# Performance work log

Measured on AMD Instinct MI355X. Metric: run time of the kernel, lower is better.

Reference implementation:

```python
import jax, jax.numpy as jnp
import numpy as np

EMBED_DIM = 1024
NUM_HEADS = 16
HEAD_DIM = EMBED_DIM // NUM_HEADS


def setup_inputs() -> dict:
    key = jax.random.key(0)
    ks = jax.random.split(key, 5)
    s = 0.02
    return {
        "x": jax.random.normal(ks[0], (2, 2048, EMBED_DIM), dtype=jnp.float32),
        "w_qkv": jax.random.normal(ks[1], (EMBED_DIM, 3 * EMBED_DIM), dtype=jnp.float32) * s,
        "b_qkv": jnp.zeros((3 * EMBED_DIM,), dtype=jnp.float32),
        "w_out": jax.random.normal(ks[2], (EMBED_DIM, EMBED_DIM), dtype=jnp.float32) * s,
        "b_out": jnp.zeros((EMBED_DIM,), dtype=jnp.float32),
    }


def reference(x, w_qkv, b_qkv, w_out, b_out):
    B, T, C = x.shape
    qkv = x @ w_qkv + b_qkv                       # [B,T,3C]
    q, k, v = jnp.split(qkv, 3, axis=-1)
    # [B,T,C] -> [B,H,T,Dh]
    def heads(t):
        return t.reshape(B, T, NUM_HEADS, HEAD_DIM).transpose(0, 2, 1, 3)
    q, k, v = heads(q), heads(k), heads(v)
    scale = 1.0 / np.sqrt(HEAD_DIM).astype(np.float32)
    scores = jnp.einsum("bhqd,bhkd->bhqk", q, k) * scale  # [B,H,T,T]
    causal = jnp.tril(jnp.ones((T, T), dtype=bool))
    scores = jnp.where(causal[None, None], scores, -jnp.inf)
    attn = jax.nn.softmax(scores, axis=-1)
    out = jnp.einsum("bhqk,bhkd->bhqd", attn, v)  # [B,H,T,Dh]
    out = out.transpose(0, 2, 1, 3).reshape(B, T, C)
    return out @ w_out + b_out
```

## Files before the change

kernel.cpp:

```cpp
#include <hip/hip_runtime.h>

typedef unsigned short u16;
typedef unsigned int u32;
typedef __attribute__((ext_vector_type(8))) short bf16x8;
typedef __attribute__((ext_vector_type(4))) float f32x4;
typedef __attribute__((ext_vector_type(16))) float f32x16;

#define TOK   4096
#define EMB   1024
#define NQKV  3072
#define TSEQ  2048
#define NH    16

__device__ __forceinline__ u16 f2b(float f) {
  union { float f; unsigned u; } v; v.f = f;
  unsigned r = v.u + 0x7FFFu + ((v.u >> 16) & 1u);
  return (u16)(r >> 16);
}

__device__ __forceinline__ u32 pack_rn(float a, float b) {
  u32 ua = __float_as_uint(a) + 0x8000u;
  u32 ub = __float_as_uint(b) + 0x8000u;
  return __builtin_amdgcn_perm(ub, ua, 0x07060302u);
}

__device__ __forceinline__ f32x16 zero16() {
  f32x16 z;
#pragma unroll
  for (int i = 0; i < 16; i++) z[i] = 0.f;
  return z;
}

__device__ __forceinline__ void gload16(const void* g, void* l) {
  __builtin_amdgcn_global_load_lds((const __attribute__((address_space(1))) void*)g,
                                   (__attribute__((address_space(3))) void*)l, 16, 0, 0);
}


__global__ __launch_bounds__(256) void prep_kernel(const float* __restrict__ x,
                                                   u16* __restrict__ x_bf,
                                                   const float* __restrict__ w_qkv,
                                                   u16* __restrict__ wqkvT,
                                                   const float* __restrict__ w_out,
                                                   u16* __restrict__ woutT) {
  __shared__ u16 sm[64][65];
  int bid = blockIdx.x, tid = threadIdx.x;
  if (bid < 4096) {
    int i = bid * 256 + tid;
    float4 v = ((const float4*)x)[i];
    union { u16 us[4]; uint2 u2; } o;
    o.us[0] = f2b(v.x); o.us[1] = f2b(v.y); o.us[2] = f2b(v.z); o.us[3] = f2b(v.w);
    ((uint2*)x_bf)[i] = o.u2;
    return;
  }
  const float* src; u16* dst; int R, C, bx, by;
  if (bid < 4096 + 768) {
    int t = bid - 4096; bx = t % 48; by = t / 48;
    src = w_qkv; dst = wqkvT; R = EMB; C = NQKV;
  } else {
    int t = bid - 4096 - 768; bx = t & 15; by = t >> 4;
    src = w_out; dst = woutT; R = EMB; C = EMB;
  }
  int c0 = bx * 64, r0 = by * 64;
#pragma unroll
  for (int i = 0; i < 16; i++) {
    int idx = tid + i * 256;
    int r = idx >> 6, c = idx & 63;
    sm[r][c] = f2b(src[(size_t)(r0 + r) * C + c0 + c]);
  }
  __syncthreads();
#pragma unroll
  for (int i = 0; i < 16; i++) {
    int idx = tid + i * 256;
    int cc = idx >> 6, rr = idx & 63;
    dst[(size_t)(c0 + cc) * R + r0 + rr] = sm[rr][cc];
  }
}

__global__ __launch_bounds__(256) void transpose_v(const u16* __restrict__ V,
                                                   u16* __restrict__ Vt) {
  __shared__ u16 sm[64][72];
  int t0 = blockIdx.x * 64, bh = blockIdx.y;
  size_t base = (size_t)bh * TSEQ * 64;
  int tid = threadIdx.x;
  int r = tid >> 2, c = (tid & 3) * 16;
  *(bf16x8*)&sm[r][c]     = *(const bf16x8*)&V[base + (size_t)(t0 + r) * 64 + c];
  *(bf16x8*)&sm[r][c + 8] = *(const bf16x8*)&V[base + (size_t)(t0 + r) * 64 + c + 8];
  __syncthreads();
  int d = tid >> 2, tc = (tid & 3) * 16;
  union { u16 us[16]; uint4 v4[2]; } o;
#pragma unroll
  for (int i = 0; i < 16; i++) o.us[i] = sm[tc + i][d];
  *(uint4*)&Vt[base + (size_t)d * TSEQ + t0 + tc]     = o.v4[0];
  *(uint4*)&Vt[base + (size_t)d * TSEQ + t0 + tc + 8] = o.v4[1];
}


template <int MODE, int TM>
__global__ __launch_bounds__(256) void gemm_bt(const u16* __restrict__ A,
                                               const u16* __restrict__ Bt,
                                               const float* __restrict__ bias,
                                               u16* __restrict__ qb, u16* __restrict__ kb,
                                               u16* __restrict__ vb, float* __restrict__ outp,
                                               int K, int N) {
  constexpr int CT = (TM == 128) ? 4 : 2;
  constexpr int RA = TM / 32;
  __shared__ u16 As[TM][64];
  __shared__ u16 Bs[128][64];
  int tid = threadIdx.x;
  int m0 = blockIdx.y * TM, n0 = blockIdx.x * 128;
  int lane = tid & 63, wid = tid >> 6;
  int wm = (TM == 128) ? (wid >> 1) * 64 : 0;
  int wn = (TM == 128) ? (wid & 1) * 64 : wid * 32;
  int l15 = lane & 15, quad = lane >> 4;
  int srow = lane >> 3, scol = (lane & 7) * 8;

  f32x4 acc[4][CT];
#pragma unroll
  for (int i = 0; i < 4; i++)
#pragma unroll
    for (int j = 0; j < CT; j++) acc[i][j] = (f32x4){0.f, 0.f, 0.f, 0.f};

  const u16* Ag = A + (size_t)(m0 + wid * (RA * 8) + srow) * K + scol;
  const u16* Bg = Bt + (size_t)(n0 + wid * 32 + srow) * K + scol;

  for (int k0 = 0; k0 < K; k0 += 64) {
#pragma unroll
    for (int i = 0; i < RA; i++)
      gload16(Ag + (size_t)(i * 8) * K + k0, &As[wid * (RA * 8) + i * 8][0]);
#pragma unroll
    for (int i = 0; i < 4; i++)
      gload16(Bg + (size_t)(i * 8) * K + k0, &Bs[wid * 32 + i * 8][0]);
    __syncthreads();

#pragma unroll
    for (int ks = 0; ks < 2; ks++) {
      bf16x8 af[4], bfr[CT];
#pragma unroll
      for (int rt = 0; rt < 4; rt++)
        af[rt] = *(const bf16x8*)&As[wm + rt * 16 + l15][ks * 32 + quad * 8];
#pragma unroll
      for (int ct = 0; ct < CT; ct++)
        bfr[ct] = *(const bf16x8*)&Bs[wn + ct * 16 + l15][ks * 32 + quad * 8];
#pragma unroll
      for (int rt = 0; rt < 4; rt++)
#pragma unroll
        for (int ct = 0; ct < CT; ct++)
          acc[rt][ct] = __builtin_amdgcn_mfma_f32_16x16x32_bf16(bfr[ct], af[rt], acc[rt][ct], 0, 0, 0);
    }
    __syncthreads();
  }

#pragma unroll
  for (int rt = 0; rt < 4; rt++) {
#pragma unroll
    for (int ct = 0; ct < CT; ct++) {
      int m = m0 + wm + rt * 16 + l15;
      int nb = n0 + wn + ct * 16 + quad * 4;
      float4 b4 = *(const float4*)&bias[nb];
      float v0 = acc[rt][ct][0] + b4.x, v1 = acc[rt][ct][1] + b4.y;
      float v2 = acc[rt][ct][2] + b4.z, v3 = acc[rt][ct][3] + b4.w;
      if (MODE == 0) {
        int sel = nb >> 10;
        int c = nb & 1023;
        int h = c >> 6, d0 = c & 63;
        int b = m >> 11, t = m & 2047;
        u16* dst = (sel == 0) ? qb : (sel == 1) ? kb : vb;
        union { u32 u[2]; uint2 u2; } o;
        o.u[0] = pack_rn(v0, v1);
        o.u[1] = pack_rn(v2, v3);
        *(uint2*)&dst[((((size_t)b * NH + h) * TSEQ + t) << 6) + d0] = o.u2;
      } else {
        float4 o = {v0, v1, v2, v3};
        *(float4*)&outp[(size_t)m * N + nb] = o;
      }
    }
  }
}


__global__ __launch_bounds__(256, 4) void attn_kernel(const u16* __restrict__ Qb,
                                                      const u16* __restrict__ Kb,
                                                      const u16* __restrict__ Vtb,
                                                      u16* __restrict__ O) {
  __shared__ u16 Ks[64][68];
  __shared__ u16 Vt[64][68];
  __shared__ float Cmb[2][16][64][2];
  __shared__ float Lmb[2][32];

  const float SCL = 0.18033688f;
  const float MOFF = 16.0f;

  int id = blockIdx.x;
  int bh = (id >> 5) & 31;
  int q5 = id & 31;
  int qt = ((id >> 8) & 1) ? (31 - q5) : q5;

  int tid = threadIdx.x, lane = tid & 63, w = tid >> 6;
  int sub = w & 1, par = w >> 1;
  int l31 = lane & 31, h = lane >> 5;
  const size_t hoff = (size_t)bh * TSEQ * 64;

  int qw = qt * 64 + sub * 32;
  int qg = qw + l31;

  bf16x8 qf[4];
  {
    const u16* qp = Qb + hoff + (size_t)qg * 64 + h * 8;
#pragma unroll
    for (int s = 0; s < 4; s++) qf[s] = *(const bf16x8*)(qp + s * 16);
  }

  f32x16 acc[2];
  acc[0] = zero16(); acc[1] = zero16();
  float l_i = 0.f;

  int r = tid >> 2, cb = (tid & 3) * 16;
  bf16x8 kr0, kr1, vr0, vr1;
  {
    const u16* kg = Kb + hoff + (size_t)r * 64 + cb;
    const u16* vg = Vtb + hoff + (size_t)r * TSEQ + cb;
    kr0 = *(const bf16x8*)kg;       kr1 = *(const bf16x8*)(kg + 8);
    vr0 = *(const bf16x8*)vg;       vr1 = *(const bf16x8*)(vg + 8);
  }

  for (int kt = 0; kt <= qt; kt++) {
    __syncthreads();
    *(bf16x8*)&Ks[r][cb]     = kr0;
    *(bf16x8*)&Ks[r][cb + 8] = kr1;
    *(bf16x8*)&Vt[r][cb]     = vr0;
    *(bf16x8*)&Vt[r][cb + 8] = vr1;
    __syncthreads();
    if (kt < qt) {
      const u16* kg = Kb + hoff + (size_t)((kt + 1) * 64 + r) * 64 + cb;
      const u16* vg = Vtb + hoff + (size_t)r * TSEQ + (kt + 1) * 64 + cb;
      kr0 = *(const bf16x8*)kg;     kr1 = *(const bf16x8*)(kg + 8);
      vr0 = *(const bf16x8*)vg;     vr1 = *(const bf16x8*)(vg + 8);
    }

    int kbt = kt * 64 + par * 32;
    if (kbt <= qw + 31) {
      f32x16 sacc = zero16();
#pragma unroll
      for (int s = 0; s < 4; s++) {
        bf16x8 kf = *(const bf16x8*)&Ks[par * 32 + l31][s * 16 + h * 8];
        sacc = __builtin_amdgcn_mfma_f32_32x32x16_bf16(kf, qf[s], sacc, 0, 0, 0);
      }

      if (kbt + 31 > qw) {
#pragma unroll
        for (int rr = 0; rr < 16; rr++) {
          int key = kbt + (rr & 3) + 8 * (rr >> 2) + 4 * h;
          if (key > qg) sacc[rr] = -1e30f;
        }
      }

#pragma unroll
      for (int rr = 0; rr < 16; rr++) {
        float p = exp2f(__builtin_fmaf(sacc[rr], SCL, -MOFF));
        sacc[rr] = p;
        l_i += p;
      }

#pragma unroll
      for (int s2 = 0; s2 < 2; s2++) {
        u32 u0 = pack_rn(sacc[8 * s2 + 0], sacc[8 * s2 + 1]);
        u32 u1 = pack_rn(sacc[8 * s2 + 2], sacc[8 * s2 + 3]);
        u32 u2 = pack_rn(sacc[8 * s2 + 4], sacc[8 * s2 + 5]);
        u32 u3 = pack_rn(sacc[8 * s2 + 6], sacc[8 * s2 + 7]);
        u32 s0 = h ? u0 : u2, s1 = h ? u1 : u3;
        u32 t0 = (u32)__shfl_xor((int)s0, 32);
        u32 t1 = (u32)__shfl_xor((int)s1, 32);
        union { u32 d[4]; bf16x8 v; } pf;
        pf.d[0] = h ? t0 : u0;
        pf.d[1] = h ? t1 : u1;
        pf.d[2] = h ? u2 : t0;
        pf.d[3] = h ? u3 : t1;
#pragma unroll
        for (int dt = 0; dt < 2; dt++) {
          bf16x8 vf = *(const bf16x8*)&Vt[dt * 32 + l31][par * 32 + s2 * 16 + h * 8];
          acc[dt] = __builtin_amdgcn_mfma_f32_32x32x16_bf16(vf, pf.v, acc[dt], 0, 0, 0);
        }
      }
    }
  }

  l_i += __shfl_xor(l_i, 32);

  __syncthreads();
  if (par == 1) {
#pragma unroll
    for (int dt = 0; dt < 2; dt++)
#pragma unroll
      for (int pr = 0; pr < 8; pr++) {
        Cmb[sub][dt * 8 + pr][lane][0] = acc[dt][2 * pr];
        Cmb[sub][dt * 8 + pr][lane][1] = acc[dt][2 * pr + 1];
      }
    if (h == 0) Lmb[sub][l31] = l_i;
  }
  __syncthreads();
  if (par == 0) {
#pragma unroll
    for (int dt = 0; dt < 2; dt++)
#pragma unroll
      for (int pr = 0; pr < 8; pr++) {
        acc[dt][2 * pr]     += Cmb[sub][dt * 8 + pr][lane][0];
        acc[dt][2 * pr + 1] += Cmb[sub][dt * 8 + pr][lane][1];
      }
    float lt = l_i + Lmb[sub][l31];
    float inv = 1.0f / lt;

    int b = bh >> 4, head = bh & 15;
    size_t rowbase = ((size_t)b * TSEQ + qg) * 1024 + head * 64;
#pragma unroll
    for (int dt = 0; dt < 2; dt++)
#pragma unroll
      for (int G = 0; G < 4; G++) {
        union { u32 u[2]; uint2 u2; } o;
        o.u[0] = pack_rn(acc[dt][4 * G + 0] * inv, acc[dt][4 * G + 1] * inv);
        o.u[1] = pack_rn(acc[dt][4 * G + 2] * inv, acc[dt][4 * G + 3] * inv);
        *(uint2*)&O[rowbase + dt * 32 + G * 8 + 4 * h] = o.u2;
      }
  }
}


extern "C" void kernel_launch(void* const* d_in, const int* in_sizes, int n_in,
                              void* d_out, int out_size, void* d_ws, size_t ws_size,
                              hipStream_t stream) {
  (void)in_sizes; (void)n_in; (void)out_size; (void)ws_size;
  const float* x     = (const float*)d_in[0];
  const float* w_qkv = (const float*)d_in[1];
  const float* b_qkv = (const float*)d_in[2];
  const float* w_out = (const float*)d_in[3];
  const float* b_out = (const float*)d_in[4];
  float* out = (float*)d_out;

  char* p = (char*)d_ws;
  u16* x_bf  = (u16*)p; p += (size_t)TOK * EMB * 2;
  u16* wqkvT = (u16*)p; p += (size_t)NQKV * EMB * 2;
  u16* woutT = (u16*)p; p += (size_t)EMB * EMB * 2;
  u16* Qb    = (u16*)p; p += (size_t)32 * TSEQ * 64 * 2;
  u16* Kb    = (u16*)p; p += (size_t)32 * TSEQ * 64 * 2;
  u16* Vraw  = (u16*)p; p += (size_t)32 * TSEQ * 64 * 2;
  u16* attn_o = (u16*)p;
  u16* Vtb   = x_bf;

  prep_kernel<<<dim3(4096 + 768 + 256), 256, 0, stream>>>(x, x_bf, w_qkv, wqkvT, w_out, woutT);
  gemm_bt<0, 128><<<dim3(NQKV / 128, TOK / 128), 256, 0, stream>>>(x_bf, wqkvT, b_qkv,
                                                                   Qb, Kb, Vraw, nullptr, EMB, NQKV);
  transpose_v<<<dim3(TSEQ / 64, 32), 256, 0, stream>>>(Vraw, Vtb);
  attn_kernel<<<dim3(1024), 256, 0, stream>>>(Qb, Kb, Vtb, attn_o);
  gemm_bt<1, 64><<<dim3(EMB / 128, TOK / 64), 256, 0, stream>>>(attn_o, woutT, b_out,
                                                                nullptr, nullptr, nullptr, out, EMB, EMB);
}
```

Before: 208.1 us.

## Double-buffer GEMM LDS tiles with XOR swizzle and unify 128x128 tiling

```diff
diff --git a/kernel.cpp b/kernel.cpp
--- a/kernel.cpp
+++ b/kernel.cpp
@@ -96,65 +96,76 @@
 }
 
 
-template <int MODE, int TM>
+template <int MODE>
 __global__ __launch_bounds__(256) void gemm_bt(const u16* __restrict__ A,
                                                const u16* __restrict__ Bt,
                                                const float* __restrict__ bias,
                                                u16* __restrict__ qb, u16* __restrict__ kb,
                                                u16* __restrict__ vb, float* __restrict__ outp,
                                                int K, int N) {
-  constexpr int CT = (TM == 128) ? 4 : 2;
-  constexpr int RA = TM / 32;
-  __shared__ u16 As[TM][64];
-  __shared__ u16 Bs[128][64];
+  __shared__ u16 As[2][128][64];
+  __shared__ u16 Bs[2][128][64];
   int tid = threadIdx.x;
-  int m0 = blockIdx.y * TM, n0 = blockIdx.x * 128;
+  int m0 = blockIdx.y * 128, n0 = blockIdx.x * 128;
   int lane = tid & 63, wid = tid >> 6;
-  int wm = (TM == 128) ? (wid >> 1) * 64 : 0;
-  int wn = (TM == 128) ? (wid & 1) * 64 : wid * 32;
+  int wm = (wid >> 1) * 64;
+  int wn = (wid & 1) * 64;
   int l15 = lane & 15, quad = lane >> 4;
-  int srow = lane >> 3, scol = (lane & 7) * 8;
-
-  f32x4 acc[4][CT];
+  int srow = lane >> 3;
+  int scol = (((lane & 7) ^ srow) * 8);
+
+  f32x4 acc[4][4];
 #pragma unroll
   for (int i = 0; i < 4; i++)
 #pragma unroll
-    for (int j = 0; j < CT; j++) acc[i][j] = (f32x4){0.f, 0.f, 0.f, 0.f};
-
-  const u16* Ag = A + (size_t)(m0 + wid * (RA * 8) + srow) * K + scol;
+    for (int j = 0; j < 4; j++) acc[i][j] = (f32x4){0.f, 0.f, 0.f, 0.f};
+
+  const u16* Ag = A + (size_t)(m0 + wid * 32 + srow) * K + scol;
   const u16* Bg = Bt + (size_t)(n0 + wid * 32 + srow) * K + scol;
 
+#pragma unroll
+  for (int i = 0; i < 4; i++)
+    gload16(Ag + (size_t)(i * 8) * K, &As[0][wid * 32 + i * 8][0]);
+#pragma unroll
+  for (int i = 0; i < 4; i++)
+    gload16(Bg + (size_t)(i * 8) * K, &Bs[0][wid * 32 + i * 8][0]);
+  __syncthreads();
+
+  int cur = 0;
   for (int k0 = 0; k0 < K; k0 += 64) {
-#pragma unroll
-    for (int i = 0; i < RA; i++)
-      gload16(Ag + (size_t)(i * 8) * K + k0, &As[wid * (RA * 8) + i * 8][0]);
-#pragma unroll
-    for (int i = 0; i < 4; i++)
-      gload16(Bg + (size_t)(i * 8) * K + k0, &Bs[wid * 32 + i * 8][0]);
+    if (k0 + 64 < K) {
+      int kn = k0 + 64;
+#pragma unroll
+      for (int i = 0; i < 4; i++)
+        gload16(Ag + (size_t)(i * 8) * K + kn, &As[cur ^ 1][wid * 32 + i * 8][0]);
+#pragma unroll
+      for (int i = 0; i < 4; i++)
+        gload16(Bg + (size_t)(i * 8) * K + kn, &Bs[cur ^ 1][wid * 32 + i * 8][0]);
+    }
+
+#pragma unroll
+    for (int ks = 0; ks < 2; ks++) {
+      bf16x8 af[4], bfr[4];
+#pragma unroll
+      for (int rt = 0; rt < 4; rt++)
+        af[rt] = *(const bf16x8*)&As[cur][wm + rt * 16 + l15][((ks * 4 + quad) ^ (l15 & 7)) * 8];
+#pragma unroll
+      for (int ct = 0; ct < 4; ct++)
+        bfr[ct] = *(const bf16x8*)&Bs[cur][wn + ct * 16 + l15][((ks * 4 + quad) ^ (l15 & 7)) * 8];
+#pragma unroll
+      for (int rt = 0; rt < 4; rt++)
+#pragma unroll
+        for (int ct = 0; ct < 4; ct++)
+          acc[rt][ct] = __builtin_amdgcn_mfma_f32_16x16x32_bf16(bfr[ct], af[rt], acc[rt][ct], 0, 0, 0);
+    }
     __syncthreads();
-
-#pragma unroll
-    for (int ks = 0; ks < 2; ks++) {
-      bf16x8 af[4], bfr[CT];
-#pragma unroll
-      for (int rt = 0; rt < 4; rt++)
-        af[rt] = *(const bf16x8*)&As[wm + rt * 16 + l15][ks * 32 + quad * 8];
-#pragma unroll
-      for (int ct = 0; ct < CT; ct++)
-        bfr[ct] = *(const bf16x8*)&Bs[wn + ct * 16 + l15][ks * 32 + quad * 8];
-#pragma unroll
-      for (int rt = 0; rt < 4; rt++)
-#pragma unroll
-        for (int ct = 0; ct < CT; ct++)
-          acc[rt][ct] = __builtin_amdgcn_mfma_f32_16x16x32_bf16(bfr[ct], af[rt], acc[rt][ct], 0, 0, 0);
-    }
-    __syncthreads();
+    cur ^= 1;
   }
 
 #pragma unroll
   for (int rt = 0; rt < 4; rt++) {
 #pragma unroll
-    for (int ct = 0; ct < CT; ct++) {
+    for (int ct = 0; ct < 4; ct++) {
       int m = m0 + wm + rt * 16 + l15;
       int nb = n0 + wn + ct * 16 + quad * 4;
       float4 b4 = *(const float4*)&bias[nb];
@@ -347,10 +358,10 @@
   u16* Vtb   = x_bf;
 
   prep_kernel<<<dim3(4096 + 768 + 256), 256, 0, stream>>>(x, x_bf, w_qkv, wqkvT, w_out, woutT);
-  gemm_bt<0, 128><<<dim3(NQKV / 128, TOK / 128), 256, 0, stream>>>(x_bf, wqkvT, b_qkv,
-                                                                   Qb, Kb, Vraw, nullptr, EMB, NQKV);
+  gemm_bt<0><<<dim3(NQKV / 128, TOK / 128), 256, 0, stream>>>(x_bf, wqkvT, b_qkv,
+                                                              Qb, Kb, Vraw, nullptr, EMB, NQKV);
   transpose_v<<<dim3(TSEQ / 64, 32), 256, 0, stream>>>(Vraw, Vtb);
   attn_kernel<<<dim3(1024), 256, 0, stream>>>(Qb, Kb, Vtb, attn_o);
-  gemm_bt<1, 64><<<dim3(EMB / 128, TOK / 64), 256, 0, stream>>>(attn_o, woutT, b_out,
-                                                                nullptr, nullptr, nullptr, out, EMB, EMB);
-}
+  gemm_bt<1><<<dim3(EMB / 128, TOK / 128), 256, 0, stream>>>(attn_o, woutT, b_out,
+                                                             nullptr, nullptr, nullptr, out, EMB, EMB);
+}
```

New measurement: 200.0 us. 3.9% less time.
